# Kernel optimization log

Hardware: AMD Instinct MI355X
Metric: run time of the kernel (lower is better)

The kernel has to match this reference:

```python
import jax, jax.numpy as jnp
import numpy as np

MAX_OBJECTS = 20
MAX_GRID = 30
LN_EPS = 1e-5


def _layernorm(x, g, b):
    m = x.mean(-1, keepdims=True)
    v = ((x - m) ** 2).mean(-1, keepdims=True)
    return (x - m) / jnp.sqrt(v + LN_EPS) * g + b


def setup_inputs() -> dict:
    key = jax.random.key(0)
    ks = jax.random.split(key, 16)
    B, ND, H, NL, NC = 16384, 16, 64, 3, 11
    OUT = MAX_GRID * MAX_GRID * NC  # 9900
    s1, s2, s64 = 1.0 / np.sqrt(ND), 1.0 / np.sqrt(2 * H), 1.0 / np.sqrt(H)
    return {
        "node_features": jax.random.normal(ks[0], (B, MAX_OBJECTS, ND), jnp.float32),
        "n_nodes": jax.random.randint(ks[1], (B,), 1, MAX_OBJECTS + 1, jnp.int32),
        "embed_w": jax.random.normal(ks[2], (ND, H), jnp.float32) * s1,
        "embed_b": jnp.zeros((H,), jnp.float32),
        "edge_w1": jax.random.normal(ks[3], (NL, 2 * H, H), jnp.float32) * s2,
        "edge_b1": jnp.zeros((NL, H), jnp.float32),
        "edge_w2": jax.random.normal(ks[4], (NL, H, H), jnp.float32) * s64,
        "edge_b2": jnp.zeros((NL, H), jnp.float32),
        "node_w1": jax.random.normal(ks[5], (NL, 2 * H, H), jnp.float32) * s2,
        "node_b1": jnp.zeros((NL, H), jnp.float32),
        "node_w2": jax.random.normal(ks[6], (NL, H, H), jnp.float32) * s64,
        "node_b2": jnp.zeros((NL, H), jnp.float32),
        "ln_g": jnp.ones((NL, H), jnp.float32),
        "ln_b": jnp.zeros((NL, H), jnp.float32),
        "ro_w1": jax.random.normal(ks[7], (H, H), jnp.float32) * s64,
        "ro_b1": jnp.zeros((H,), jnp.float32),
        "ro_w2": jax.random.normal(ks[8], (H, OUT), jnp.float32) * s64,
        "ro_b2": jnp.zeros((OUT,), jnp.float32),
    }


def reference(node_features, n_nodes, embed_w, embed_b,
              edge_w1, edge_b1, edge_w2, edge_b2,
              node_w1, node_b1, node_w2, node_b2,
              ln_g, ln_b, ro_w1, ro_b1, ro_w2, ro_b2):
    B = node_features.shape[0]
    h = node_features @ embed_w + embed_b  # (B, 20, H)
    # mask is identical across layers (n_nodes is fixed)
    mask = (jnp.arange(MAX_OBJECTS)[None, :] < n_nodes[:, None]).astype(h.dtype)[..., None]  # (B,20,1)
    cnt = jnp.clip(mask.sum(1, keepdims=True), 1.0, None)  # (B,1,1)
    n_layers = edge_w1.shape[0]
    for i in range(n_layers):
        msg_mean = (h * mask).sum(1, keepdims=True) / cnt  # (B,1,H)
        msg_mean = jnp.broadcast_to(msg_mean, h.shape)
        edge_in = jnp.concatenate([h, msg_mean], -1)  # (B,20,2H)
        edge_msg = jax.nn.relu(edge_in @ edge_w1[i] + edge_b1[i]) @ edge_w2[i] + edge_b2[i]
        node_in = jnp.concatenate([h, edge_msg], -1)
        h = h + (jax.nn.relu(node_in @ node_w1[i] + node_b1[i]) @ node_w2[i] + node_b2[i])
        h = _layernorm(h, ln_g[i], ln_b[i])
        h = h * mask
    graph_vec = (h * mask).sum(1) / jnp.clip(mask.sum(1), 1.0, None)  # (B,H)
    out = jax.nn.relu(graph_vec @ ro_w1 + ro_b1) @ ro_w2 + ro_b2  # (B, 9900)
    n_colors = out.shape[-1] // (MAX_GRID * MAX_GRID)
    return out.reshape(B, MAX_GRID, MAX_GRID, n_colors).transpose(0, 3, 1, 2)
```

## Files before the change

kernel.cpp:

```cpp
#include <hip/hip_runtime.h>
#include <hip/hip_bf16.h>
#include <stdint.h>

typedef __attribute__((ext_vector_type(8))) short bf16x8;
typedef __attribute__((ext_vector_type(4))) float f32x4;

__device__ __forceinline__ uint32_t f2bfu(float x){
  union { float f; uint32_t u; } v; v.f = x;
  return (v.u + 0x7FFFu + ((v.u >> 16) & 1u)) >> 16;
}
__device__ __forceinline__ short f2bf(float x){ return (short)(uint16_t)f2bfu(x); }
__device__ __forceinline__ uint32_t pk2(float a, float b){
  return (f2bfu(a) & 0xFFFFu) | (f2bfu(b) << 16);
}

__device__ __forceinline__ f32x4 mfma16(bf16x8 a, bf16x8 b, f32x4 c){
  return __builtin_amdgcn_mfma_f32_16x16x32_bf16(a, b, c, 0, 0, 0);
}

__global__ void prep_fold(const float* __restrict__ ew2, const float* __restrict__ eb2,
                          const float* __restrict__ nw1, const float* __restrict__ nb1,
                          float* __restrict__ wfold, float* __restrict__ bfold)
{
  int l = blockIdx.x, t = threadIdx.x;
  const float* A  = ew2 + l*4096;
  const float* Bm = nw1 + l*8192 + 4096;
  for (int i = 0; i < 16; ++i){
    int idx = t + i*256;
    int r = idx >> 6, c = idx & 63;
    float s = 0.f;
    for (int m = 0; m < 64; ++m) s += A[r*64 + m] * Bm[m*64 + c];
    wfold[l*4096 + idx] = s;
  }
  if (t < 64){
    float s = nb1[l*64 + t];
    const float* e2 = eb2 + l*64;
    for (int m = 0; m < 64; ++m) s += e2[m] * Bm[m*64 + t];
    bfold[l*64 + t] = s;
  }
}

__global__ void prep_pack(const float* __restrict__ embw,
                          const float* __restrict__ ew1,
                          const float* __restrict__ nw1,
                          const float* __restrict__ nw2,
                          const float* __restrict__ row1,
                          const float* __restrict__ wfold,
                          short* __restrict__ wpk)
{
  int tid = blockIdx.x*256 + threadIdx.x;
  if (tid >= 67584) return;
  int rem; const float* Wa; const float* Wb = nullptr; int Kact;
  if (tid < 2048){ rem = tid; Wa = embw; Kact = 16; }
  else if (tid < 63488){
    int t2 = tid - 2048, li = t2/20480, r = t2%20480;
    if (r < 8192)       { rem = r;         Wa = ew1 + li*8192; Wb = Wa + 4096;        Kact = 128; }
    else if (r < 16384) { rem = r - 8192;  Wa = nw1 + li*8192; Wb = wfold + li*4096;  Kact = 128; }
    else                { rem = r - 16384; Wa = nw2 + li*4096;                         Kact = 64; }
  } else { rem = tid - 63488; Wa = row1; Kact = 64; }
  int e = rem & 7, lane = (rem >> 3) & 63, mt = (rem >> 9) & 3, ks = rem >> 11;
  int k = ks*32 + (lane >> 4)*8 + e;
  int col = mt*16 + (lane & 15);
  float v = 0.f;
  if (k < Kact) v = (k < 64) ? Wa[k*64 + col] : Wb[(k - 64)*64 + col];
  wpk[tid] = f2bf(v);
}

__global__ void prep_w2(const float* __restrict__ ro_w2, const float* __restrict__ ro_b2,
                        short* __restrict__ w2p, float* __restrict__ b2p)
{
  int tid = blockIdx.x * 256 + threadIdx.x;
  if (tid < 634880){
    int e = tid & 7, lane = (tid >> 3) & 63, ks = (tid >> 9) & 1, j = (tid >> 10) & 3, g = tid >> 12;
    int k = ks*32 + (lane >> 4)*8 + e;
    int p = g*64 + (lane & 15)*4 + j;
    float v = 0.f;
    if (p < 9900){ int c = p / 900, rm = p % 900; v = ro_w2[k*9900 + rm*11 + c]; }
    w2p[tid] = f2bf(v);
  } else if (tid < 634880 + 9920){
    int p = tid - 634880;
    float v = 0.f;
    if (p < 9900){ int c = p / 900, rm = p % 900; v = ro_b2[rm*11 + c]; }
    b2p[p] = v;
  }
}

__global__ __launch_bounds__(256) void gnn_phaseA(
    const float* __restrict__ nf, const int* __restrict__ nn,
    const float* __restrict__ embb,
    const float* __restrict__ eb1, const float* __restrict__ nb2,
    const float* __restrict__ lng, const float* __restrict__ lnb,
    const short* __restrict__ wpk, const float* __restrict__ bfold,
    short* __restrict__ gvb)
{
  __shared__ short lds[4][4160];
  const int wave = threadIdx.x >> 6, lane = threadIdx.x & 63;
  const int l15 = lane & 15, lg = lane >> 4;
  const int b = blockIdx.x * 4 + wave;
  short* hs  = &lds[wave][0];
  short* buf = &lds[wave][2048];
  short* mms = &lds[wave][4096];
  const int n = nn[b];
  const float cinv = 1.0f / (float)(n < 1 ? 1 : n);
  const bool keep0 = l15 < n, keep1 = (16 + l15) < n;
  const int fb = lg*4;
  const int sw = (l15 & 7) << 3;
  const int rb0 = l15*64, rb1 = (16 + l15)*64;

  float hD[4][2][4];
  f32x4 acc[4][2];
  float cs[4][4];

  {
    bf16x8 bfr[2];
#pragma unroll
    for (int nt = 0; nt < 2; ++nt){
      int node = nt*16 + l15;
      bf16x8 a;
#pragma unroll
      for (int e = 0; e < 8; ++e) a[e] = 0;
      if (lg < 2 && node < 20){
        const float* s = nf + (b*20 + node)*16 + lg*8;
        float4 s0 = *(const float4*)(s);
        float4 s1 = *(const float4*)(s + 4);
        union { bf16x8 v; uint32_t u[4]; } q;
        q.u[0] = pk2(s0.x, s0.y); q.u[1] = pk2(s0.z, s0.w);
        q.u[2] = pk2(s1.x, s1.y); q.u[3] = pk2(s1.z, s1.w);
        a = q.v;
      }
      bfr[nt] = a;
    }
#pragma unroll
    for (int mt = 0; mt < 4; ++mt){
      bf16x8 af = *(const bf16x8*)(wpk + (mt*64 + lane)*8);
      f32x4 z = {0.f,0.f,0.f,0.f};
      acc[mt][0] = mfma16(af, bfr[0], z);
      acc[mt][1] = mfma16(af, bfr[1], z);
    }
#pragma unroll
    for (int mt = 0; mt < 4; ++mt){
      float4 bias = *(const float4*)(embb + mt*16 + fb);
#pragma unroll
      for (int nt = 0; nt < 2; ++nt){
        bool kp = nt ? keep1 : keep0;
#pragma unroll
        for (int e = 0; e < 4; ++e){
          float v = acc[mt][nt][e] + ((const float*)&bias)[e];
          hD[mt][nt][e] = kp ? v : 0.f;
        }
        int base = nt ? rb1 : rb0;
        uint32_t w0 = pk2(hD[mt][nt][0], hD[mt][nt][1]);
        uint32_t w1 = pk2(hD[mt][nt][2], hD[mt][nt][3]);
        *(uint2*)&hs[base + ((mt*16 + fb) ^ sw)] = make_uint2(w0, w1);
      }
#pragma unroll
      for (int e = 0; e < 4; ++e){
        float c = hD[mt][0][e] + hD[mt][1][e];
        c += __shfl_xor(c, 1); c += __shfl_xor(c, 2);
        c += __shfl_xor(c, 4); c += __shfl_xor(c, 8);
        cs[mt][e] = c * cinv;
      }
    }
    if (l15 == 0){
#pragma unroll
      for (int mt = 0; mt < 4; ++mt)
        *(uint2*)&mms[mt*16 + fb] = make_uint2(pk2(cs[mt][0], cs[mt][1]),
                                               pk2(cs[mt][2], cs[mt][3]));
    }
  }

  for (int li = 0; li < 3; ++li){
    const short* wl = wpk + 2048 + li*20480;

#pragma unroll
    for (int mt = 0; mt < 4; ++mt){ acc[mt][0] = (f32x4){0.f,0.f,0.f,0.f}; acc[mt][1] = (f32x4){0.f,0.f,0.f,0.f}; }
#pragma unroll
    for (int ks = 0; ks < 4; ++ks){
      bf16x8 bfr0, bfr1;
      if (ks < 2){
        int ko = (ks*32 + lg*8) ^ sw;
        bfr0 = *(const bf16x8*)&hs[rb0 + ko];
        bfr1 = *(const bf16x8*)&hs[rb1 + ko];
      } else {
        bfr0 = *(const bf16x8*)&mms[(ks - 2)*32 + lg*8];
        bfr1 = bfr0;
      }
#pragma unroll
      for (int mt = 0; mt < 4; ++mt){
        bf16x8 af = *(const bf16x8*)(wl + ((ks*4 + mt)*64 + lane)*8);
        acc[mt][0] = mfma16(af, bfr0, acc[mt][0]);
        acc[mt][1] = mfma16(af, bfr1, acc[mt][1]);
      }
    }
#pragma unroll
    for (int mt = 0; mt < 4; ++mt){
      float4 bias = *(const float4*)(eb1 + li*64 + mt*16 + fb);
#pragma unroll
      for (int nt = 0; nt < 2; ++nt){
        float v0 = acc[mt][nt][0] + ((const float*)&bias)[0];
        float v1 = acc[mt][nt][1] + ((const float*)&bias)[1];
        float v2 = acc[mt][nt][2] + ((const float*)&bias)[2];
        float v3 = acc[mt][nt][3] + ((const float*)&bias)[3];
        v0 = v0 > 0.f ? v0 : 0.f; v1 = v1 > 0.f ? v1 : 0.f;
        v2 = v2 > 0.f ? v2 : 0.f; v3 = v3 > 0.f ? v3 : 0.f;
        int base = nt ? rb1 : rb0;
        *(uint2*)&buf[base + ((mt*16 + fb) ^ sw)] = make_uint2(pk2(v0, v1), pk2(v2, v3));
      }
    }

#pragma unroll
    for (int mt = 0; mt < 4; ++mt){ acc[mt][0] = (f32x4){0.f,0.f,0.f,0.f}; acc[mt][1] = (f32x4){0.f,0.f,0.f,0.f}; }
#pragma unroll
    for (int ks = 0; ks < 4; ++ks){
      const short* src = (ks < 2) ? hs : buf;
      int ko = (((ks & 1)*32) + lg*8) ^ sw;
      bf16x8 bfr0 = *(const bf16x8*)&src[rb0 + ko];
      bf16x8 bfr1 = *(const bf16x8*)&src[rb1 + ko];
#pragma unroll
      for (int mt = 0; mt < 4; ++mt){
        bf16x8 af = *(const bf16x8*)(wl + 8192 + ((ks*4 + mt)*64 + lane)*8);
        acc[mt][0] = mfma16(af, bfr0, acc[mt][0]);
        acc[mt][1] = mfma16(af, bfr1, acc[mt][1]);
      }
    }
#pragma unroll
    for (int mt = 0; mt < 4; ++mt){
      float4 bias = *(const float4*)(bfold + li*64 + mt*16 + fb);
#pragma unroll
      for (int nt = 0; nt < 2; ++nt){
        float v0 = acc[mt][nt][0] + ((const float*)&bias)[0];
        float v1 = acc[mt][nt][1] + ((const float*)&bias)[1];
        float v2 = acc[mt][nt][2] + ((const float*)&bias)[2];
        float v3 = acc[mt][nt][3] + ((const float*)&bias)[3];
        v0 = v0 > 0.f ? v0 : 0.f; v1 = v1 > 0.f ? v1 : 0.f;
        v2 = v2 > 0.f ? v2 : 0.f; v3 = v3 > 0.f ? v3 : 0.f;
        int base = nt ? rb1 : rb0;
        *(uint2*)&buf[base + ((mt*16 + fb) ^ sw)] = make_uint2(pk2(v0, v1), pk2(v2, v3));
      }
    }

#pragma unroll
    for (int mt = 0; mt < 4; ++mt){ acc[mt][0] = (f32x4){0.f,0.f,0.f,0.f}; acc[mt][1] = (f32x4){0.f,0.f,0.f,0.f}; }
#pragma unroll
    for (int ks = 0; ks < 2; ++ks){
      int ko = (ks*32 + lg*8) ^ sw;
      bf16x8 bfr0 = *(const bf16x8*)&buf[rb0 + ko];
      bf16x8 bfr1 = *(const bf16x8*)&buf[rb1 + ko];
#pragma unroll
      for (int mt = 0; mt < 4; ++mt){
        bf16x8 af = *(const bf16x8*)(wl + 16384 + ((ks*4 + mt)*64 + lane)*8);
        acc[mt][0] = mfma16(af, bfr0, acc[mt][0]);
        acc[mt][1] = mfma16(af, bfr1, acc[mt][1]);
      }
    }
    float s1a = 0.f, s2a = 0.f, s1b = 0.f, s2b = 0.f;
#pragma unroll
    for (int mt = 0; mt < 4; ++mt){
      float4 bias = *(const float4*)(nb2 + li*64 + mt*16 + fb);
#pragma unroll
      for (int e = 0; e < 4; ++e){
        float va = hD[mt][0][e] + acc[mt][0][e] + ((const float*)&bias)[e];
        float vb = hD[mt][1][e] + acc[mt][1][e] + ((const float*)&bias)[e];
        hD[mt][0][e] = va; hD[mt][1][e] = vb;
        s1a += va; s2a += va*va; s1b += vb; s2b += vb*vb;
      }
    }
    s1a += __shfl_xor(s1a, 16); s1a += __shfl_xor(s1a, 32);
    s2a += __shfl_xor(s2a, 16); s2a += __shfl_xor(s2a, 32);
    s1b += __shfl_xor(s1b, 16); s1b += __shfl_xor(s1b, 32);
    s2b += __shfl_xor(s2b, 16); s2b += __shfl_xor(s2b, 32);
    float meana = s1a * 0.015625f, meanb = s1b * 0.015625f;
    float rstda = rsqrtf(s2a * 0.015625f - meana*meana + 1e-5f);
    float rstdb = rsqrtf(s2b * 0.015625f - meanb*meanb + 1e-5f);
#pragma unroll
    for (int mt = 0; mt < 4; ++mt){
      float4 g = *(const float4*)(lng + li*64 + mt*16 + fb);
      float4 bb = *(const float4*)(lnb + li*64 + mt*16 + fb);
#pragma unroll
      for (int e = 0; e < 4; ++e){
        float ge = ((const float*)&g)[e], be = ((const float*)&bb)[e];
        float ya = (hD[mt][0][e] - meana) * rstda * ge + be;
        float yb = (hD[mt][1][e] - meanb) * rstdb * ge + be;
        ya = keep0 ? ya : 0.f;
        yb = keep1 ? yb : 0.f;
        hD[mt][0][e] = ya; hD[mt][1][e] = yb;
        cs[mt][e] = ya + yb;
      }
      *(uint2*)&hs[rb0 + ((mt*16 + fb) ^ sw)] =
          make_uint2(pk2(hD[mt][0][0], hD[mt][0][1]), pk2(hD[mt][0][2], hD[mt][0][3]));
      *(uint2*)&hs[rb1 + ((mt*16 + fb) ^ sw)] =
          make_uint2(pk2(hD[mt][1][0], hD[mt][1][1]), pk2(hD[mt][1][2], hD[mt][1][3]));
    }
#pragma unroll
    for (int mt = 0; mt < 4; ++mt)
#pragma unroll
      for (int e = 0; e < 4; ++e){
        float c = cs[mt][e];
        c += __shfl_xor(c, 1); c += __shfl_xor(c, 2);
        c += __shfl_xor(c, 4); c += __shfl_xor(c, 8);
        cs[mt][e] = c * cinv;
      }
    if (l15 == 0){
      if (li < 2){
#pragma unroll
        for (int mt = 0; mt < 4; ++mt)
          *(uint2*)&mms[mt*16 + fb] = make_uint2(pk2(cs[mt][0], cs[mt][1]),
                                                 pk2(cs[mt][2], cs[mt][3]));
      } else {
#pragma unroll
        for (int mt = 0; mt < 4; ++mt)
          *(uint2*)(gvb + b*64 + mt*16 + fb) = make_uint2(pk2(cs[mt][0], cs[mt][1]),
                                                          pk2(cs[mt][2], cs[mt][3]));
      }
    }
  }
}

__global__ __launch_bounds__(256) void gnn_phaseB(
    const short* __restrict__ gvb, const float* __restrict__ rb1,
    const short* __restrict__ wro1, const short* __restrict__ w2p,
    const float* __restrict__ b2p, float* __restrict__ out)
{
  __shared__ short tl[4][1024];
  const int wave = threadIdx.x >> 6, lane = threadIdx.x & 63;
  const int l15 = lane & 15, lg = lane >> 4;
  const int b0 = blockIdx.x * 64 + wave * 16;

  f32x4 tacc[4];
#pragma unroll
  for (int nt = 0; nt < 4; ++nt) tacc[nt] = (f32x4){0.f,0.f,0.f,0.f};
#pragma unroll
  for (int ks = 0; ks < 2; ++ks){
    bf16x8 a = *(const bf16x8*)&gvb[(b0 + l15)*64 + ks*32 + lg*8];
#pragma unroll
    for (int nt = 0; nt < 4; ++nt){
      bf16x8 bq = *(const bf16x8*)(wro1 + ((ks*4 + nt)*64 + lane)*8);
      tacc[nt] = mfma16(a, bq, tacc[nt]);
    }
  }
  short* tw = tl[wave];
#pragma unroll
  for (int nt = 0; nt < 4; ++nt){
    float bias = rb1[nt*16 + l15];
#pragma unroll
    for (int e = 0; e < 4; ++e){
      int row = lg*4 + e;
      float v = tacc[nt][e] + bias;
      v = v > 0.f ? v : 0.f;
      tw[((row*64) + (nt*16 + l15)) ^ ((row & 7) << 3)] = f2bf(v);
    }
  }
  bf16x8 ta0 = *(const bf16x8*)&tw[((l15*64) + (lg*8))      ^ ((l15 & 7) << 3)];
  bf16x8 ta1 = *(const bf16x8*)&tw[((l15*64) + (32 + lg*8)) ^ ((l15 & 7) << 3)];

  const int g0 = blockIdx.y * 31;
  const int g1 = (g0 + 31 < 155) ? g0 + 31 : 155;
  for (int g = g0; g < g1; ++g){
    const bf16x8* wp = (const bf16x8*)w2p + g*512;
    f32x4 c[4];
#pragma unroll
    for (int j = 0; j < 4; ++j){
      f32x4 z = {0.f,0.f,0.f,0.f};
      z = mfma16(ta0, wp[(j*2 + 0)*64 + lane], z);
      c[j] = mfma16(ta1, wp[(j*2 + 1)*64 + lane], z);
    }
    int p0 = g*64 + l15*4;
    if (p0 < 9900){
      float4 bias = *(const float4*)(b2p + p0);
      float* o = out + (size_t)(b0 + lg*4)*9900 + p0;
#pragma unroll
      for (int e = 0; e < 4; ++e){
        float4 o4 = make_float4(c[0][e] + bias.x, c[1][e] + bias.y,
                                c[2][e] + bias.z, c[3][e] + bias.w);
        *(float4*)(o + (size_t)e*9900) = o4;
      }
    }
  }
}

extern "C" void kernel_launch(void* const* d_in, const int* in_sizes, int n_in,
                              void* d_out, int out_size, void* d_ws, size_t ws_size,
                              hipStream_t stream)
{
  const float* nf   = (const float*)d_in[0];
  const int*   nn   = (const int*)d_in[1];
  const float* embw = (const float*)d_in[2];
  const float* embb = (const float*)d_in[3];
  const float* ew1  = (const float*)d_in[4];
  const float* eb1  = (const float*)d_in[5];
  const float* ew2  = (const float*)d_in[6];
  const float* eb2  = (const float*)d_in[7];
  const float* nw1  = (const float*)d_in[8];
  const float* nb1  = (const float*)d_in[9];
  const float* nw2  = (const float*)d_in[10];
  const float* nb2  = (const float*)d_in[11];
  const float* lng  = (const float*)d_in[12];
  const float* lnb  = (const float*)d_in[13];
  const float* rw1  = (const float*)d_in[14];
  const float* rb1  = (const float*)d_in[15];
  const float* rw2  = (const float*)d_in[16];
  const float* rb2  = (const float*)d_in[17];
  float* out = (float*)d_out;

  const int B = in_sizes[0] / 320;

  char* ws = (char*)d_ws;
  short* gvb  = (short*)ws;
  float* b2p  = (float*)(ws + 2097152);
  float* wfold= (float*)(ws + 2136832);
  float* bfold= (float*)(ws + 2185984);
  short* wpk  = (short*)(ws + 2186752);
  short* w2p  = (short*)(ws + 2321920);

  prep_fold<<<3, 256, 0, stream>>>(ew2, eb2, nw1, nb1, wfold, bfold);
  prep_pack<<<(67584 + 255)/256, 256, 0, stream>>>(embw, ew1, nw1, nw2, rw1, wfold, wpk);
  prep_w2<<<(634880 + 9920 + 255)/256, 256, 0, stream>>>(rw2, rb2, w2p, b2p);
  gnn_phaseA<<<B/4, 256, 0, stream>>>(nf, nn, embb, eb1, nb2, lng, lnb, wpk, bfold, gvb);
  gnn_phaseB<<<dim3(B/64, 5), 256, 0, stream>>>(gvb, rb1, wpk + 63488, w2p, b2p, out);
}
```

Baseline: 493.1 us.

## Double rows per wave in readout and enlarge phaseA blocks with barriers

The readout kernel now has each wave handle 32 batch rows instead of 16, so every loaded packed ro_w2 fragment feeds twice as many MFMAs and weight traffic per output drops by half. PhaseA moves to 512-thread blocks with eight waves each, and adds block-wide __syncthreads before each GEMM stage, apparently to keep waves in lockstep so they share weight fetches through the cache. The readout change raises register pressure and halves the grid in x. The added barriers in phaseA are not needed for correctness since each wave uses its own LDS slice, so they may cost stall time.

```diff
diff --git a/kernel.cpp b/kernel.cpp
--- a/kernel.cpp
+++ b/kernel.cpp
@@ -85,7 +85,7 @@
   }
 }
 
-__global__ __launch_bounds__(256) void gnn_phaseA(
+__global__ __launch_bounds__(512) void gnn_phaseA(
     const float* __restrict__ nf, const int* __restrict__ nn,
     const float* __restrict__ embb,
     const float* __restrict__ eb1, const float* __restrict__ nb2,
@@ -93,10 +93,10 @@
     const short* __restrict__ wpk, const float* __restrict__ bfold,
     short* __restrict__ gvb)
 {
-  __shared__ short lds[4][4160];
+  __shared__ short lds[8][4160];
   const int wave = threadIdx.x >> 6, lane = threadIdx.x & 63;
   const int l15 = lane & 15, lg = lane >> 4;
-  const int b = blockIdx.x * 4 + wave;
+  const int b = blockIdx.x * 8 + wave;
   short* hs  = &lds[wave][0];
   short* buf = &lds[wave][2048];
   short* mms = &lds[wave][4096];
@@ -130,6 +130,7 @@
       }
       bfr[nt] = a;
     }
+    __syncthreads();
 #pragma unroll
     for (int mt = 0; mt < 4; ++mt){
       bf16x8 af = *(const bf16x8*)(wpk + (mt*64 + lane)*8);
@@ -172,6 +173,7 @@
   for (int li = 0; li < 3; ++li){
     const short* wl = wpk + 2048 + li*20480;
 
+    __syncthreads();
 #pragma unroll
     for (int mt = 0; mt < 4; ++mt){ acc[mt][0] = (f32x4){0.f,0.f,0.f,0.f}; acc[mt][1] = (f32x4){0.f,0.f,0.f,0.f}; }
 #pragma unroll
@@ -208,6 +210,7 @@
       }
     }
 
+    __syncthreads();
 #pragma unroll
     for (int mt = 0; mt < 4; ++mt){ acc[mt][0] = (f32x4){0.f,0.f,0.f,0.f}; acc[mt][1] = (f32x4){0.f,0.f,0.f,0.f}; }
 #pragma unroll
@@ -239,6 +242,7 @@
       }
     }
 
+    __syncthreads();
 #pragma unroll
     for (int mt = 0; mt < 4; ++mt){ acc[mt][0] = (f32x4){0.f,0.f,0.f,0.f}; acc[mt][1] = (f32x4){0.f,0.f,0.f,0.f}; }
 #pragma unroll
@@ -321,58 +325,72 @@
     const short* __restrict__ wro1, const short* __restrict__ w2p,
     const float* __restrict__ b2p, float* __restrict__ out)
 {
-  __shared__ short tl[4][1024];
+  __shared__ short tl[4][2048];
   const int wave = threadIdx.x >> 6, lane = threadIdx.x & 63;
   const int l15 = lane & 15, lg = lane >> 4;
-  const int b0 = blockIdx.x * 64 + wave * 16;
-
-  f32x4 tacc[4];
-#pragma unroll
-  for (int nt = 0; nt < 4; ++nt) tacc[nt] = (f32x4){0.f,0.f,0.f,0.f};
+  const int b0 = blockIdx.x * 128 + wave * 32;
+
+  f32x4 tacc[2][4];
+#pragma unroll
+  for (int rt = 0; rt < 2; ++rt)
+#pragma unroll
+    for (int nt = 0; nt < 4; ++nt) tacc[rt][nt] = (f32x4){0.f,0.f,0.f,0.f};
 #pragma unroll
   for (int ks = 0; ks < 2; ++ks){
-    bf16x8 a = *(const bf16x8*)&gvb[(b0 + l15)*64 + ks*32 + lg*8];
+    bf16x8 a0 = *(const bf16x8*)&gvb[(size_t)(b0 + l15)*64 + ks*32 + lg*8];
+    bf16x8 a1 = *(const bf16x8*)&gvb[(size_t)(b0 + 16 + l15)*64 + ks*32 + lg*8];
 #pragma unroll
     for (int nt = 0; nt < 4; ++nt){
       bf16x8 bq = *(const bf16x8*)(wro1 + ((ks*4 + nt)*64 + lane)*8);
-      tacc[nt] = mfma16(a, bq, tacc[nt]);
+      tacc[0][nt] = mfma16(a0, bq, tacc[0][nt]);
+      tacc[1][nt] = mfma16(a1, bq, tacc[1][nt]);
     }
   }
   short* tw = tl[wave];
 #pragma unroll
-  for (int nt = 0; nt < 4; ++nt){
-    float bias = rb1[nt*16 + l15];
-#pragma unroll
-    for (int e = 0; e < 4; ++e){
-      int row = lg*4 + e;
-      float v = tacc[nt][e] + bias;
-      v = v > 0.f ? v : 0.f;
-      tw[((row*64) + (nt*16 + l15)) ^ ((row & 7) << 3)] = f2bf(v);
-    }
-  }
-  bf16x8 ta0 = *(const bf16x8*)&tw[((l15*64) + (lg*8))      ^ ((l15 & 7) << 3)];
-  bf16x8 ta1 = *(const bf16x8*)&tw[((l15*64) + (32 + lg*8)) ^ ((l15 & 7) << 3)];
+  for (int rt = 0; rt < 2; ++rt)
+#pragma unroll
+    for (int nt = 0; nt < 4; ++nt){
+      float bias = rb1[nt*16 + l15];
+#pragma unroll
+      for (int e = 0; e < 4; ++e){
+        int row = rt*16 + lg*4 + e;
+        float v = tacc[rt][nt][e] + bias;
+        v = v > 0.f ? v : 0.f;
+        tw[((row*64) + (nt*16 + l15)) ^ ((row & 7) << 3)] = f2bf(v);
+      }
+    }
+  bf16x8 ta[2][2];
+  ta[0][0] = *(const bf16x8*)&tw[((l15*64) + (lg*8))           ^ ((l15 & 7) << 3)];
+  ta[0][1] = *(const bf16x8*)&tw[((l15*64) + (32 + lg*8))      ^ ((l15 & 7) << 3)];
+  ta[1][0] = *(const bf16x8*)&tw[(((16+l15)*64) + (lg*8))      ^ ((l15 & 7) << 3)];
+  ta[1][1] = *(const bf16x8*)&tw[(((16+l15)*64) + (32 + lg*8)) ^ ((l15 & 7) << 3)];
 
   const int g0 = blockIdx.y * 31;
   const int g1 = (g0 + 31 < 155) ? g0 + 31 : 155;
   for (int g = g0; g < g1; ++g){
     const bf16x8* wp = (const bf16x8*)w2p + g*512;
-    f32x4 c[4];
+    f32x4 c[2][4];
 #pragma unroll
     for (int j = 0; j < 4; ++j){
-      f32x4 z = {0.f,0.f,0.f,0.f};
-      z = mfma16(ta0, wp[(j*2 + 0)*64 + lane], z);
-      c[j] = mfma16(ta1, wp[(j*2 + 1)*64 + lane], z);
+      bf16x8 w0 = wp[(j*2 + 0)*64 + lane];
+      bf16x8 w1 = wp[(j*2 + 1)*64 + lane];
+      f32x4 z0 = {0.f,0.f,0.f,0.f}, z1 = {0.f,0.f,0.f,0.f};
+      z0 = mfma16(ta[0][0], w0, z0); c[0][j] = mfma16(ta[0][1], w1, z0);
+      z1 = mfma16(ta[1][0], w0, z1); c[1][j] = mfma16(ta[1][1], w1, z1);
     }
     int p0 = g*64 + l15*4;
     if (p0 < 9900){
       float4 bias = *(const float4*)(b2p + p0);
-      float* o = out + (size_t)(b0 + lg*4)*9900 + p0;
-#pragma unroll
-      for (int e = 0; e < 4; ++e){
-        float4 o4 = make_float4(c[0][e] + bias.x, c[1][e] + bias.y,
-                                c[2][e] + bias.z, c[3][e] + bias.w);
-        *(float4*)(o + (size_t)e*9900) = o4;
+#pragma unroll
+      for (int rt = 0; rt < 2; ++rt){
+        float* o = out + (size_t)(b0 + rt*16 + lg*4)*9900 + p0;
+#pragma unroll
+        for (int e = 0; e < 4; ++e){
+          float4 o4 = make_float4(c[rt][0][e] + bias.x, c[rt][1][e] + bias.y,
+                                  c[rt][2][e] + bias.z, c[rt][3][e] + bias.w);
+          *(float4*)(o + (size_t)e*9900) = o4;
+        }
       }
     }
   }
@@ -415,6 +433,6 @@
   prep_fold<<<3, 256, 0, stream>>>(ew2, eb2, nw1, nb1, wfold, bfold);
   prep_pack<<<(67584 + 255)/256, 256, 0, stream>>>(embw, ew1, nw1, nw2, rw1, wfold, wpk);
   prep_w2<<<(634880 + 9920 + 255)/256, 256, 0, stream>>>(rw2, rb2, w2p, b2p);
-  gnn_phaseA<<<B/4, 256, 0, stream>>>(nf, nn, embb, eb1, nb2, lng, lnb, wpk, bfold, gvb);
-  gnn_phaseB<<<dim3(B/64, 5), 256, 0, stream>>>(gvb, rb1, wpk + 63488, w2p, b2p, out);
-}
+  gnn_phaseA<<<B/8, 512, 0, stream>>>(nf, nn, embb, eb1, nb2, lng, lnb, wpk, bfold, gvb);
+  gnn_phaseB<<<dim3(B/128, 5), 256, 0, stream>>>(gvb, rb1, wpk + 63488, w2p, b2p, out);
+}
```

Result: no change. 485.8 us (-1.5%).
